# Kernel optimization log

Hardware: AMD Instinct MI355X
Metric: run time of the kernel (lower is better)

Reference implementation:

```python
import jax, jax.numpy as jnp
import numpy as np

B, S, H, T, DI, HID, K, HEADS = 8, 1024, 768, 8, 64, 128, 8, 2
NEG = 1.0e12


def _build_adj(spans):
    # spans: [K,3] int; returns [K+1,K+1] edge multiplicity matrix (dst, src)
    s, e = spans[:, 0], spans[:, 1]
    same = (s[:, None] == s[None, :]) & (e[:, None] == e[None, :])
    # contain[i,j]: span i strictly contains span j (source appends this edge twice)
    contain = (s[:, None] <= s[None, :]) & (e[None, :] <= e[:, None]) & (~same)
    N = K + 1
    adj = jnp.eye(N, dtype=jnp.float32)                    # PyG add_self_loops
    adj = adj.at[1:, 0].add(1.0)                           # global -> span i
    adj = adj.at[0, 1:].add(1.0)                           # span i -> global
    adj = adj.at[1:, 1:].add(2.0 * contain.T.astype(jnp.float32))
    return adj


def _gat(x, adj, W, a_src, a_dst, b):
    # x [N,F]; adj [N,N] multiplicity with layout (dst, src). PyG GATConv math.
    N = x.shape[0]
    h = (x @ W).reshape(N, HEADS, -1)                      # [N,Hd,D]
    asrc = jnp.einsum('nhd,hd->nh', h, a_src)
    adst = jnp.einsum('nhd,hd->nh', h, a_dst)
    ee = jax.nn.leaky_relu(adst[:, None, :] + asrc[None, :, :], 0.2)  # [dst,src,Hd]
    logmult = jnp.where(adj > 0, jnp.log(jnp.maximum(adj, 1e-20)), 0.0)
    scores = jnp.where(adj[:, :, None] > 0, ee + logmult[:, :, None], -1e30)
    attn = jax.nn.softmax(scores, axis=1)                  # softmax over source nodes
    out = jnp.einsum('dsh,shf->dhf', attn, h).reshape(N, -1)
    return out + b


def _layernorm(x, g, bta):
    mu = x.mean(-1, keepdims=True)
    var = x.var(-1, keepdims=True)
    return (x - mu) / jnp.sqrt(var + 1e-5) * g + bta


def _forward(hidden, attention_mask, spans, W1, a_src1, a_dst1, b1, ln_g, ln_b,
             W2, a_src2, a_dst2, b2, dense_W, dense_b,
             g_centers, g_sigmas, g_weights, corr):
    start, end, etype = spans[..., 0], spans[..., 1], spans[..., 2]  # [B,K]
    pos = jnp.arange(S)
    span_mask = ((pos[None, None, :] >= start[..., None]) &
                 (pos[None, None, :] <= end[..., None])).astype(hidden.dtype)  # [B,K,S]
    span_len = (end - start + 1).astype(hidden.dtype)
    span_feat = jnp.einsum('bks,bsh->bkh', span_mask, hidden) / span_len[..., None]
    global_feat = hidden.mean(axis=1, keepdims=True)                 # [B,1,H]
    nodes = jnp.concatenate([global_feat, span_feat], axis=1)        # [B,K+1,H]
    adj = jax.vmap(_build_adj)(spans)                                # [B,K+1,K+1]

    g1 = jax.vmap(lambda x, a: _gat(x, a, W1, a_src1, a_dst1, b1))(nodes, adj)
    g1 = _layernorm(jax.nn.relu(g1), ln_g, ln_b)
    g2 = jax.vmap(lambda x, a: _gat(x, a, W2, a_src2, a_dst2, b2))(g1, adj)
    g2 = jax.nn.relu(g2)
    enhanced = g2.mean(axis=1)                                       # per-graph mean pool [B,2*HID]

    cover = span_mask.sum(axis=1)                                    # [B,S] how many spans cover token s
    token_enh = cover[..., None] * enhanced[:, None, :]              # [B,S,2*HID]
    combined = jnp.concatenate([hidden, token_enh], axis=-1)

    qk = (combined @ dense_W + dense_b).reshape(B, S, T, 2 * DI)
    qw, kw = qk[..., :DI], qk[..., DI:]

    # RoPE (sin/cos interleaved exactly as in source)
    inv = jnp.power(10000.0, -2.0 * jnp.arange(DI // 2) / DI)
    ang = pos[:, None].astype(jnp.float32) * inv[None, :]            # [S,DI/2]
    sin = jnp.repeat(jnp.sin(ang), 2, axis=-1)[None, :, None, :]     # [1,S,1,DI]
    cos = jnp.repeat(jnp.cos(ang), 2, axis=-1)[None, :, None, :]

    def rot(v):
        v2 = jnp.stack([-v[..., 1::2], v[..., ::2]], axis=-1).reshape(v.shape)
        return v * cos + v2 * sin

    qw, kw = rot(qw), rot(kw)

    logits = jnp.einsum('bmtd,bntd->btmn', qw, kw)                   # [B,T,S,S]

    # multi-modal gaussian kernel span maps (vectorized over batch/span/component)
    pf = pos.astype(jnp.float32)
    dxs = pf[None, None, None, :] - start[..., None, None] - g_centers[None, None, :, None]
    dxe = pf[None, None, None, :] - end[..., None, None] - g_centers[None, None, :, None]
    Ksr = g_weights[None, None, :, None] * jnp.exp(-0.5 * (dxs / g_sigmas[None, None, :, None]) ** 2)
    Ken = g_weights[None, None, :, None] * jnp.exp(-0.5 * (dxe / g_sigmas[None, None, :, None]) ** 2)
    gmap = jnp.einsum('bkcm,bkcn->bkmn', Ksr, Ken)                   # [B,K,S,S]
    corr_span = corr[etype]                                          # [B,K,T]
    logits = logits + jnp.einsum('bkt,bkmn->btmn', corr_span, gmap)

    pad = attention_mask[:, None, None, :]                           # key-dim-only mask (as in source)
    logits = logits * pad - (1.0 - pad) * NEG
    tril = jnp.tril(jnp.ones((S, S), logits.dtype), -1)
    logits = logits - tril * NEG
    return logits / jnp.sqrt(jnp.float32(DI))


def setup_inputs() -> dict:
    key = jax.random.key(0)
    ks = jax.random.split(key, 16)
    hidden = jax.random.normal(ks[0], (B, S, H), jnp.float32)
    attention_mask = jnp.ones((B, S), jnp.float32)
    start = jax.random.randint(ks[1], (B, K), 0, S - 32)
    length = jax.random.randint(ks[2], (B, K), 1, 16)
    spans = jnp.stack([start, start + length,
                       jax.random.randint(ks[3], (B, K), 0, T)], axis=-1).astype(jnp.int32)
    sd = 0.05
    return {
        'hidden': hidden,
        'attention_mask': attention_mask,
        'spans': spans,
        'W1': jax.random.normal(ks[4], (H, HEADS * HID), jnp.float32) * sd,
        'a_src1': jax.random.normal(ks[5], (HEADS, HID), jnp.float32) * sd,
        'a_dst1': jax.random.normal(ks[6], (HEADS, HID), jnp.float32) * sd,
        'b1': jnp.zeros((HEADS * HID,), jnp.float32),
        'ln_g': jnp.ones((HEADS * HID,), jnp.float32),
        'ln_b': jnp.zeros((HEADS * HID,), jnp.float32),
        'W2': jax.random.normal(ks[7], (HEADS * HID, HEADS * HID), jnp.float32) * sd,
        'a_src2': jax.random.normal(ks[8], (HEADS, HID), jnp.float32) * sd,
        'a_dst2': jax.random.normal(ks[9], (HEADS, HID), jnp.float32) * sd,
        'b2': jnp.zeros((HEADS * HID,), jnp.float32),
        'dense_W': jax.random.normal(ks[10], (H + HEADS * HID, T * 2 * DI), jnp.float32) * sd,
        'dense_b': jnp.zeros((T * 2 * DI,), jnp.float32),
        'g_centers': jnp.array([0.0, 0.0], jnp.float32),
        'g_sigmas': jnp.array([1.0, 3.0], jnp.float32),
        'g_weights': jnp.array([0.5, 0.5], jnp.float32),
        'corr': jnp.eye(T, dtype=jnp.float32),
    }


def reference(hidden, attention_mask, spans, W1, a_src1, a_dst1, b1, ln_g, ln_b,
              W2, a_src2, a_dst2, b2, dense_W, dense_b,
              g_centers, g_sigmas, g_weights, corr):
    return _forward(hidden, attention_mask, spans, W1, a_src1, a_dst1, b1, ln_g, ln_b,
                    W2, a_src2, a_dst2, b2, dense_W, dense_b,
                    g_centers, g_sigmas, g_weights, corr)
```

## Files before the change

### kernel.cpp

```cpp
#include <hip/hip_runtime.h>
#include <cstdint>
#include <cstddef>

#define BB 8
#define SS 1024
#define HH 768
#define TT 8
#define DII 64
#define HIDD 128
#define KSP 8
#define NHEADS 2
#define NNODES 9
#define GDIM 256
#define CDIM 1024
#define DAUGP 96
#define NEGV 1e12f

using bf16x8 = __attribute__((ext_vector_type(8))) __bf16;
using f32x4  = __attribute__((ext_vector_type(4))) float;

static __device__ inline unsigned short f2bf(float x) {
  union { float f; unsigned u; } v; v.f = x;
  unsigned r = v.u + 0x7fff + ((v.u >> 16) & 1);
  return (unsigned short)(r >> 16);
}

__global__ __launch_bounds__(256) void kprep(
    const float* __restrict__ hidden, const float* __restrict__ dense_W,
    const int* __restrict__ spans, const float* __restrict__ corr,
    const float* __restrict__ gc, const float* __restrict__ gs,
    const float* __restrict__ gw,
    unsigned short* __restrict__ hbf, unsigned short* __restrict__ WtopT,
    float* __restrict__ part, float* __restrict__ nodes, float* __restrict__ cover,
    unsigned short* __restrict__ Qa, unsigned short* __restrict__ Ka) {
  int blk = blockIdx.x, tid = threadIdx.x;
  if (blk < 128) {
    int z = blk & 15, b = blk >> 4;
    const float* hb = hidden + (size_t)b * SS * HH;
    unsigned short* ho = hbf + (size_t)b * SS * HH;
    #pragma unroll
    for (int j = 0; j < 3; j++) {
      int c = tid + j * 256;
      float acc = 0.f;
      #pragma unroll 8
      for (int r = z * 64; r < z * 64 + 64; r++) {
        float v = hb[(size_t)r * HH + c];
        ho[(size_t)r * HH + c] = f2bf(v);
        acc += v;
      }
      part[((size_t)b * 16 + z) * HH + c] = acc;
    }
  } else if (blk < 192) {
    int q = blk - 128;
    int k = q & 7, b = q >> 3;
    __shared__ int sp[KSP * 3];
    if (tid < KSP * 3) sp[tid] = spans[b * KSP * 3 + tid];
    __syncthreads();
    if (tid < 128) {
      int s = k * 128 + tid;
      float c = 0.f;
      #pragma unroll
      for (int kk = 0; kk < KSP; kk++)
        c += (s >= sp[kk * 3] && s <= sp[kk * 3 + 1]) ? 1.f : 0.f;
      cover[b * SS + s] = c;
    }
    int st = sp[k * 3], en = sp[k * 3 + 1];
    float inv = 1.f / (float)(en - st + 1);
    const float* hb = hidden + (size_t)b * SS * HH;
    #pragma unroll
    for (int ci = 0; ci < 3; ci++) {
      int c = tid + ci * 256;
      float a = 0.f;
      #pragma unroll
      for (int j = 0; j < 16; j++) {
        int s = st + j;
        int sc = (s <= en) ? s : en;
        float v = hb[(size_t)sc * HH + c];
        a += (s <= en) ? v : 0.f;
      }
      nodes[((size_t)b * NNODES + (k + 1)) * HH + c] = a * inv;
    }
  } else if (blk < 960) {
    __shared__ float t[32][33];
    int q = blk - 192;
    int k0 = (q % 24) * 32, n0 = (q / 24) * 32;
    int r = tid >> 3, c4 = (tid & 7) * 4;
    float4 v = *(const float4*)&dense_W[(size_t)(k0 + r) * CDIM + n0 + c4];
    t[r][c4 + 0] = v.x; t[r][c4 + 1] = v.y; t[r][c4 + 2] = v.z; t[r][c4 + 3] = v.w;
    __syncthreads();
    int ro = tid >> 3, co4 = (tid & 7) * 4;
    ushort4 o;
    o.x = f2bf(t[co4 + 0][ro]); o.y = f2bf(t[co4 + 1][ro]);
    o.z = f2bf(t[co4 + 2][ro]); o.w = f2bf(t[co4 + 3][ro]);
    *(ushort4*)&WtopT[(size_t)(n0 + ro) * HH + k0 + co4] = o;
  } else {
    int g = tid >> 5, lane = tid & 31;
    int row = (blk - 960) * 8 + g;
    int b = row >> 10, s = row & 1023;
    int j = lane & 15;
    int kp = j >> 1, c = j & 1;
    int st = spans[(b * KSP + kp) * 3 + 0];
    int en = spans[(b * KSP + kp) * 3 + 1];
    int et = spans[(b * KSP + kp) * 3 + 2];
    float sig = gs[c], wgt = gw[c], ce = gc[c];
    if (lane < 16) {
      float dx = ((float)(s - st) - ce) / sig;
      float e = wgt * __expf(-0.5f * dx * dx);
      #pragma unroll
      for (int t = 0; t < TT; t++) {
        size_t base = ((size_t)(b * TT + t) * SS + s) * DAUGP;
        Qa[base + 64 + j] = f2bf(corr[et * TT + t] * e);
        Qa[base + 80 + j] = 0;
      }
    } else {
      float dx = ((float)(s - en) - ce) / sig;
      unsigned short bv = f2bf(wgt * __expf(-0.5f * dx * dx));
      #pragma unroll
      for (int t = 0; t < TT; t++) {
        size_t base = ((size_t)(b * TT + t) * SS + s) * DAUGP;
        Ka[base + 64 + j] = bv;
        Ka[base + 80 + j] = 0;
      }
    }
  }
}

__global__ __launch_bounds__(512) void k2_gat(
    const float* __restrict__ part, const float* __restrict__ nodes_g,
    const int* __restrict__ spans,
    const float* __restrict__ W1, const float* __restrict__ a_src1,
    const float* __restrict__ a_dst1, const float* __restrict__ b1,
    const float* __restrict__ ln_g, const float* __restrict__ ln_b,
    const float* __restrict__ W2, const float* __restrict__ a_src2,
    const float* __restrict__ a_dst2, const float* __restrict__ b2,
    float* __restrict__ enhg) {
  int b = blockIdx.x, tid = threadIdx.x;
  __shared__ __align__(16) float nod[NNODES * HH];
  __shared__ __align__(16) float hbuf[NNODES * GDIM];
  __shared__ __align__(16) float gbuf[NNODES * GDIM];
  __shared__ __align__(16) float pbuf[2 * NNODES * GDIM];
  __shared__ float asrc[NNODES * NHEADS], adst[NNODES * NHEADS];
  __shared__ float adjm[NNODES * NNODES];
  __shared__ float attn[NNODES * NNODES * NHEADS];
  __shared__ float mu_s[NNODES], rs_s[NNODES];
  __shared__ int sp[KSP * 3];
  if (tid < KSP * 3) sp[tid] = spans[b * KSP * 3 + tid];
  for (int c = tid; c < HH; c += 512) {
    float s = 0.f;
    #pragma unroll
    for (int z = 0; z < 16; z++) s += part[((size_t)b * 16 + z) * HH + c];
    nod[c] = s * (1.f / (float)SS);
  }
  for (int i = tid; i < (NNODES - 1) * HH; i += 512)
    nod[HH + i] = nodes_g[(size_t)b * NNODES * HH + HH + i];
  __syncthreads();
  {
    int col = tid & 255, h = tid >> 8;
    float acc[NNODES];
    #pragma unroll
    for (int n = 0; n < NNODES; n++) acc[n] = 0.f;
    int dlo = h * 384;
    #pragma unroll 2
    for (int d0 = dlo; d0 < dlo + 384; d0 += 4) {
      float4 nv[NNODES];
      #pragma unroll
      for (int n = 0; n < NNODES; n++) nv[n] = *(const float4*)&nod[n * HH + d0];
      float w0 = W1[(size_t)(d0 + 0) * GDIM + col];
      float w1 = W1[(size_t)(d0 + 1) * GDIM + col];
      float w2 = W1[(size_t)(d0 + 2) * GDIM + col];
      float w3 = W1[(size_t)(d0 + 3) * GDIM + col];
      #pragma unroll
      for (int n = 0; n < NNODES; n++)
        acc[n] += nv[n].x * w0 + nv[n].y * w1 + nv[n].z * w2 + nv[n].w * w3;
    }
    #pragma unroll
    for (int n = 0; n < NNODES; n++) pbuf[(h * NNODES + n) * GDIM + col] = acc[n];
  }
  __syncthreads();
  if (tid < GDIM) {
    #pragma unroll
    for (int n = 0; n < NNODES; n++)
      hbuf[n * GDIM + tid] = pbuf[n * GDIM + tid] + pbuf[(NNODES + n) * GDIM + tid];
  } else if (tid < 256 + NNODES * NNODES) {
    int q = tid - 256;
    int i = q / NNODES, j = q % NNODES;
    float a = (i == j) ? 1.f : 0.f;
    if (i > 0 && j == 0) a += 1.f;
    if (i == 0 && j > 0) a += 1.f;
    if (i > 0 && j > 0 && i != j) {
      int x = j - 1, y = i - 1;
      int sx = sp[x * 3], ex = sp[x * 3 + 1], sy = sp[y * 3], ey = sp[y * 3 + 1];
      bool same = (sx == sy) && (ex == ey);
      if (sx <= sy && ey <= ex && !same) a += 2.f;
    }
    adjm[q] = a;
  }
  __syncthreads();
  if (tid < NNODES * NHEADS) {
    int n = tid >> 1, hd = tid & 1;
    float sa = 0.f, sd = 0.f;
    #pragma unroll 8
    for (int f = 0; f < HIDD; f++) {
      float v = hbuf[n * GDIM + hd * HIDD + f];
      sa += v * a_src1[hd * HIDD + f];
      sd += v * a_dst1[hd * HIDD + f];
    }
    asrc[tid] = sa; adst[tid] = sd;
  }
  __syncthreads();
  if (tid < NNODES * NHEADS) {
    int d = tid >> 1, hd = tid & 1;
    float sc[NNODES]; float mx = -1e30f;
    for (int s2 = 0; s2 < NNODES; s2++) {
      float a = adjm[d * NNODES + s2]; float v;
      if (a > 0.f) {
        float e = adst[d * 2 + hd] + asrc[s2 * 2 + hd];
        e = (e > 0.f) ? e : 0.2f * e;
        v = e + __logf(a);
      } else v = -1e30f;
      sc[s2] = v; mx = fmaxf(mx, v);
    }
    float ssum = 0.f;
    for (int s2 = 0; s2 < NNODES; s2++) { float ex = __expf(sc[s2] - mx); sc[s2] = ex; ssum += ex; }
    float inv = 1.f / ssum;
    for (int s2 = 0; s2 < NNODES; s2++) attn[(d * NNODES + s2) * NHEADS + hd] = sc[s2] * inv;
  }
  __syncthreads();
  if (tid < 256) {
    int hd = tid >> 7;
    float bbv = b1[tid];
    for (int d = 0; d < NNODES; d++) {
      float acc = bbv;
      #pragma unroll
      for (int s2 = 0; s2 < NNODES; s2++)
        acc += attn[(d * NNODES + s2) * NHEADS + hd] * hbuf[s2 * GDIM + tid];
      gbuf[d * GDIM + tid] = fmaxf(acc, 0.f);
    }
  }
  __syncthreads();
  if (tid < NNODES) {
    float s1 = 0.f, s2v = 0.f;
    #pragma unroll 8
    for (int o = 0; o < GDIM; o++) { float v = gbuf[tid * GDIM + o]; s1 += v; s2v += v * v; }
    float mu = s1 / (float)GDIM;
    float var = s2v / (float)GDIM - mu * mu;
    mu_s[tid] = mu; rs_s[tid] = rsqrtf(var + 1e-5f);
  }
  __syncthreads();
  if (tid < 256) {
    float g = ln_g[tid], bt = ln_b[tid];
    for (int d = 0; d < NNODES; d++)
      gbuf[d * GDIM + tid] = (gbuf[d * GDIM + tid] - mu_s[d]) * rs_s[d] * g + bt;
  }
  __syncthreads();
  {
    int col = tid & 255, h = tid >> 8;
    float acc[NNODES];
    #pragma unroll
    for (int n = 0; n < NNODES; n++) acc[n] = 0.f;
    int dlo = h * 128;
    #pragma unroll 2
    for (int d0 = dlo; d0 < dlo + 128; d0 += 4) {
      float4 nv[NNODES];
      #pragma unroll
      for (int n = 0; n < NNODES; n++) nv[n] = *(const float4*)&gbuf[n * GDIM + d0];
      float w0 = W2[(size_t)(d0 + 0) * GDIM + col];
      float w1 = W2[(size_t)(d0 + 1) * GDIM + col];
      float w2 = W2[(size_t)(d0 + 2) * GDIM + col];
      float w3 = W2[(size_t)(d0 + 3) * GDIM + col];
      #pragma unroll
      for (int n = 0; n < NNODES; n++)
        acc[n] += nv[n].x * w0 + nv[n].y * w1 + nv[n].z * w2 + nv[n].w * w3;
    }
    #pragma unroll
    for (int n = 0; n < NNODES; n++) pbuf[(h * NNODES + n) * GDIM + col] = acc[n];
  }
  __syncthreads();
  if (tid < GDIM) {
    #pragma unroll
    for (int n = 0; n < NNODES; n++)
      hbuf[n * GDIM + tid] = pbuf[n * GDIM + tid] + pbuf[(NNODES + n) * GDIM + tid];
  }
  __syncthreads();
  if (tid < NNODES * NHEADS) {
    int n = tid >> 1, hd = tid & 1;
    float sa = 0.f, sd = 0.f;
    #pragma unroll 8
    for (int f = 0; f < HIDD; f++) {
      float v = hbuf[n * GDIM + hd * HIDD + f];
      sa += v * a_src2[hd * HIDD + f];
      sd += v * a_dst2[hd * HIDD + f];
    }
    asrc[tid] = sa; adst[tid] = sd;
  }
  __syncthreads();
  if (tid < NNODES * NHEADS) {
    int d = tid >> 1, hd = tid & 1;
    float sc[NNODES]; float mx = -1e30f;
    for (int s2 = 0; s2 < NNODES; s2++) {
      float a = adjm[d * NNODES + s2]; float v;
      if (a > 0.f) {
        float e = adst[d * 2 + hd] + asrc[s2 * 2 + hd];
        e = (e > 0.f) ? e : 0.2f * e;
        v = e + __logf(a);
      } else v = -1e30f;
      sc[s2] = v; mx = fmaxf(mx, v);
    }
    float ssum = 0.f;
    for (int s2 = 0; s2 < NNODES; s2++) { float ex = __expf(sc[s2] - mx); sc[s2] = ex; ssum += ex; }
    float inv = 1.f / ssum;
    for (int s2 = 0; s2 < NNODES; s2++) attn[(d * NNODES + s2) * NHEADS + hd] = sc[s2] * inv;
  }
  __syncthreads();
  if (tid < 256) {
    int hd = tid >> 7;
    float bbv = b2[tid];
    float msum = 0.f;
    for (int d = 0; d < NNODES; d++) {
      float acc = bbv;
      #pragma unroll
      for (int s2 = 0; s2 < NNODES; s2++)
        acc += attn[(d * NNODES + s2) * NHEADS + hd] * hbuf[s2 * GDIM + tid];
      msum += fmaxf(acc, 0.f);
    }
    enhg[b * GDIM + tid] = msum / 9.f;
  }
}

__global__ void k2b_e2(const float* __restrict__ enhg, const float* __restrict__ dense_W,
                       float* __restrict__ E2) {
  int b = blockIdx.y, tid = threadIdx.x;
  int o = blockIdx.x * 256 + tid;
  __shared__ __align__(16) float eh[GDIM];
  eh[tid] = enhg[b * GDIM + tid];
  __syncthreads();
  float acc = 0.f;
  #pragma unroll 2
  for (int d = 0; d < GDIM; d += 4) {
    float4 ev = *(const float4*)&eh[d];
    acc += ev.x * dense_W[(size_t)(HH + d + 0) * CDIM + o];
    acc += ev.y * dense_W[(size_t)(HH + d + 1) * CDIM + o];
    acc += ev.z * dense_W[(size_t)(HH + d + 2) * CDIM + o];
    acc += ev.w * dense_W[(size_t)(HH + d + 3) * CDIM + o];
  }
  E2[b * CDIM + o] = acc;
}

__global__ __launch_bounds__(256) void k3_dense(
    const unsigned short* __restrict__ hbf, const unsigned short* __restrict__ WtopT,
    const float* __restrict__ dense_b, const float* __restrict__ cover,
    const float* __restrict__ E2,
    unsigned short* __restrict__ Qa, unsigned short* __restrict__ Ka) {
  __shared__ unsigned short As[128 * 40];
  __shared__ unsigned short Bs[128 * 40];
  int tid = threadIdx.x;
  int n0 = blockIdx.x * 128, m0 = blockIdx.y * 128;
  int wave = tid >> 6, lane = tid & 63;
  int wr = wave >> 1, wc = wave & 1;
  int colL = lane & 15, quad = lane >> 4;
  f32x4 acc[4][4];
  #pragma unroll
  for (int i = 0; i < 4; i++)
    #pragma unroll
    for (int j = 0; j < 4; j++) { acc[i][j][0] = 0.f; acc[i][j][1] = 0.f; acc[i][j][2] = 0.f; acc[i][j][3] = 0.f; }
  for (int k0 = 0; k0 < HH; k0 += 32) {
    uint4 va[2], vb[2];
    #pragma unroll
    for (int it = 0; it < 2; it++) {
      int idx = tid + it * 256;
      int r = idx >> 2, seg = idx & 3;
      va[it] = *(const uint4*)(hbf + (size_t)(m0 + r) * HH + k0 + seg * 8);
      vb[it] = *(const uint4*)(WtopT + (size_t)(n0 + r) * HH + k0 + seg * 8);
    }
    __syncthreads();
    #pragma unroll
    for (int it = 0; it < 2; it++) {
      int idx = tid + it * 256;
      int r = idx >> 2, seg = idx & 3;
      *(uint4*)&As[r * 40 + seg * 8] = va[it];
      *(uint4*)&Bs[r * 40 + seg * 8] = vb[it];
    }
    __syncthreads();
    bf16x8 af[4], bf[4];
    #pragma unroll
    for (int tm = 0; tm < 4; tm++)
      af[tm] = *(const bf16x8*)&As[(wr * 64 + tm * 16 + colL) * 40 + quad * 8];
    #pragma unroll
    for (int tn = 0; tn < 4; tn++)
      bf[tn] = *(const bf16x8*)&Bs[(wc * 64 + tn * 16 + colL) * 40 + quad * 8];
    #pragma unroll
    for (int tm = 0; tm < 4; tm++)
      #pragma unroll
      for (int tn = 0; tn < 4; tn++)
        acc[tm][tn] = __builtin_amdgcn_mfma_f32_16x16x32_bf16(af[tm], bf[tn], acc[tm][tn], 0, 0, 0);
  }
  int b = m0 >> 10;
  const float LOG1E4_32 = 0.28782313662425576f;
  unsigned short* __restrict__ dst = (wc == 0) ? Qa : Ka;
  #pragma unroll
  for (int tn = 0; tn < 4; tn++) {
    int col = n0 + wc * 64 + tn * 16 + colL;
    float e2 = E2[b * CDIM + col];
    float db = dense_b[col];
    int t = col >> 7;
    int dd = tn * 16 + colL;
    int i0 = dd >> 1;
    float inv = __expf(-(float)i0 * LOG1E4_32);
    float sgn = (dd & 1) ? 1.f : -1.f;
    size_t tbase = (size_t)(b * TT + t) * SS;
    #pragma unroll
    for (int tm = 0; tm < 4; tm++) {
      int rbase = m0 + wr * 64 + tm * 16 + quad * 4;
      #pragma unroll
      for (int r = 0; r < 4; r++) {
        int m = rbase + r;
        int s = m & 1023;
        float w = acc[tm][tn][r] + cover[m] * e2 + db;
        float p = __shfl_xor(w, 1, 64);
        float sn, cs;
        __sincosf((float)s * inv, &sn, &cs);
        float o = w * cs + sgn * p * sn;
        dst[(tbase + s) * DAUGP + dd] = f2bf(o);
      }
    }
  }
}

__global__ __launch_bounds__(256) void k5_logits(
    const unsigned short* __restrict__ Qa, const unsigned short* __restrict__ Ka,
    const float* __restrict__ amask, float* __restrict__ out) {
  int bz = blockIdx.z; int b = bz >> 3;
  int n0 = blockIdx.x * 128, m0 = blockIdx.y * 128;
  int tid = threadIdx.x;
  if (n0 + 127 < m0) {
    int r0 = tid >> 5, c4 = (tid & 31) * 4;
    float4 pv = *(const float4*)&amask[b * SS + n0 + c4];
    float4 o;
    o.x = (-(1.f - pv.x) * NEGV - NEGV) * 0.125f;
    o.y = (-(1.f - pv.y) * NEGV - NEGV) * 0.125f;
    o.z = (-(1.f - pv.z) * NEGV - NEGV) * 0.125f;
    o.w = (-(1.f - pv.w) * NEGV - NEGV) * 0.125f;
    for (int r = r0; r < 128; r += 8)
      *(float4*)&out[((size_t)bz * SS + m0 + r) * SS + n0 + c4] = o;
    return;
  }
  __shared__ unsigned short Qs[128 * 104];
  __shared__ unsigned short Ks[128 * 104];
  const unsigned short* Qrow = Qa + ((size_t)bz * SS + m0) * DAUGP;
  const unsigned short* Krow = Ka + ((size_t)bz * SS + n0) * DAUGP;
  #pragma unroll
  for (int it = 0; it < 6; it++) {
    int idx = tid + it * 256;
    int r = idx / 12, seg = idx % 12;
    uint4 vq = *(const uint4*)(Qrow + (size_t)r * DAUGP + seg * 8);
    uint4 vk = *(const uint4*)(Krow + (size_t)r * DAUGP + seg * 8);
    *(uint4*)&Qs[r * 104 + seg * 8] = vq;
    *(uint4*)&Ks[r * 104 + seg * 8] = vk;
  }
  __syncthreads();
  int wave = tid >> 6, lane = tid & 63;
  int wr = wave >> 1, wc = wave & 1;
  int colL = lane & 15, quad = lane >> 4;
  f32x4 acc[4][4];
  #pragma unroll
  for (int i = 0; i < 4; i++)
    #pragma unroll
    for (int j = 0; j < 4; j++) { acc[i][j][0] = 0.f; acc[i][j][1] = 0.f; acc[i][j][2] = 0.f; acc[i][j][3] = 0.f; }
  #pragma unroll
  for (int ks = 0; ks < 3; ks++) {
    bf16x8 af[4], bf[4];
    #pragma unroll
    for (int tm = 0; tm < 4; tm++)
      af[tm] = *(const bf16x8*)&Qs[(wr * 64 + tm * 16 + colL) * 104 + ks * 32 + quad * 8];
    #pragma unroll
    for (int tn = 0; tn < 4; tn++)
      bf[tn] = *(const bf16x8*)&Ks[(wc * 64 + tn * 16 + colL) * 104 + ks * 32 + quad * 8];
    #pragma unroll
    for (int tm = 0; tm < 4; tm++)
      #pragma unroll
      for (int tn = 0; tn < 4; tn++)
        acc[tm][tn] = __builtin_amdgcn_mfma_f32_16x16x32_bf16(af[tm], bf[tn], acc[tm][tn], 0, 0, 0);
  }
  #pragma unroll
  for (int tn = 0; tn < 4; tn++) {
    int col = n0 + wc * 64 + tn * 16 + colL;
    float p = amask[b * SS + col];
    float negp = -(1.f - p) * NEGV;
    #pragma unroll
    for (int tm = 0; tm < 4; tm++) {
      int rbase = m0 + wr * 64 + tm * 16 + quad * 4;
      #pragma unroll
      for (int r = 0; r < 4; r++) {
        int m = rbase + r;
        float v = acc[tm][tn][r] * p + negp;
        if (col < m) v -= NEGV;
        out[((size_t)bz * SS + m) * SS + col] = v * 0.125f;
      }
    }
  }
}

extern "C" void kernel_launch(void* const* d_in, const int* in_sizes, int n_in,
                              void* d_out, int out_size, void* d_ws, size_t ws_size,
                              hipStream_t stream) {
  const float* hidden  = (const float*)d_in[0];
  const float* amask   = (const float*)d_in[1];
  const int*   spans   = (const int*)d_in[2];
  const float* W1      = (const float*)d_in[3];
  const float* a_src1  = (const float*)d_in[4];
  const float* a_dst1  = (const float*)d_in[5];
  const float* b1      = (const float*)d_in[6];
  const float* ln_g    = (const float*)d_in[7];
  const float* ln_b    = (const float*)d_in[8];
  const float* W2      = (const float*)d_in[9];
  const float* a_src2  = (const float*)d_in[10];
  const float* a_dst2  = (const float*)d_in[11];
  const float* b2      = (const float*)d_in[12];
  const float* dense_W = (const float*)d_in[13];
  const float* dense_b = (const float*)d_in[14];
  const float* gc      = (const float*)d_in[15];
  const float* gs      = (const float*)d_in[16];
  const float* gw      = (const float*)d_in[17];
  const float* corr    = (const float*)d_in[18];

  char* wsb = (char*)d_ws;
  unsigned short* hbf  = (unsigned short*)wsb;                wsb += (size_t)BB * SS * HH * 2;
  unsigned short* WtopT= (unsigned short*)wsb;                wsb += (size_t)CDIM * HH * 2;
  unsigned short* Qa   = (unsigned short*)wsb;                wsb += (size_t)BB * TT * SS * DAUGP * 2;
  unsigned short* Ka   = (unsigned short*)wsb;                wsb += (size_t)BB * TT * SS * DAUGP * 2;
  float* nodes         = (float*)wsb;                         wsb += (size_t)BB * NNODES * HH * 4;
  float* cover         = (float*)wsb;                         wsb += (size_t)BB * SS * 4;
  float* E2            = (float*)wsb;                         wsb += (size_t)BB * CDIM * 4;
  float* enhg          = (float*)wsb;                         wsb += (size_t)BB * GDIM * 4;
  float* part          = (float*)wsb;                         wsb += (size_t)BB * 16 * HH * 4;
  float* outp = (float*)d_out;

  kprep<<<1984, 256, 0, stream>>>(hidden, dense_W, spans, corr, gc, gs, gw,
                                  hbf, WtopT, part, nodes, cover, Qa, Ka);
  k2_gat<<<BB, 512, 0, stream>>>(part, nodes, spans, W1, a_src1, a_dst1, b1, ln_g, ln_b,
                                 W2, a_src2, a_dst2, b2, enhg);
  k2b_e2<<<dim3(CDIM / 256, BB), 256, 0, stream>>>(enhg, dense_W, E2);
  k3_dense<<<dim3(CDIM / 128, (BB * SS) / 128), 256, 0, stream>>>(hbf, WtopT, dense_b,
                                                                  cover, E2, Qa, Ka);
  k5_logits<<<dim3(8, 8, BB * TT), 256, 0, stream>>>(Qa, Ka, amask, outp);
}
```

Baseline: 554.6 us.

## Stage logits tile through LDS for coalesced stores; widen GAT block to 1024 threads

The logits kernel now writes each 64x128 half of its output tile into shared memory, reusing the Q/K staging buffer, and then stores it with contiguous float4 row writes. Before, each lane scattered scalar stores along the MFMA accumulator layout. The GAT kernel also doubles its block to 1024 threads and splits both projection reductions four ways, adding more partial sums to combine. The change costs extra barriers and an LDS round trip in the logits epilogue, in exchange for better-coalesced writes of the large output.

New measurement: 556.3 us. About the same (+0.3%).

```diff
diff --git a/kernel.cpp b/kernel.cpp
--- a/kernel.cpp
+++ b/kernel.cpp
@@ -125,7 +125,7 @@
   }
 }
 
-__global__ __launch_bounds__(512) void k2_gat(
+__global__ __launch_bounds__(1024) void k2_gat(
     const float* __restrict__ part, const float* __restrict__ nodes_g,
     const int* __restrict__ spans,
     const float* __restrict__ W1, const float* __restrict__ a_src1,
@@ -138,30 +138,30 @@
   __shared__ __align__(16) float nod[NNODES * HH];
   __shared__ __align__(16) float hbuf[NNODES * GDIM];
   __shared__ __align__(16) float gbuf[NNODES * GDIM];
-  __shared__ __align__(16) float pbuf[2 * NNODES * GDIM];
+  __shared__ __align__(16) float pbuf[4 * NNODES * GDIM];
   __shared__ float asrc[NNODES * NHEADS], adst[NNODES * NHEADS];
   __shared__ float adjm[NNODES * NNODES];
   __shared__ float attn[NNODES * NNODES * NHEADS];
   __shared__ float mu_s[NNODES], rs_s[NNODES];
   __shared__ int sp[KSP * 3];
   if (tid < KSP * 3) sp[tid] = spans[b * KSP * 3 + tid];
-  for (int c = tid; c < HH; c += 512) {
+  for (int c = tid; c < HH; c += 1024) {
     float s = 0.f;
     #pragma unroll
     for (int z = 0; z < 16; z++) s += part[((size_t)b * 16 + z) * HH + c];
     nod[c] = s * (1.f / (float)SS);
   }
-  for (int i = tid; i < (NNODES - 1) * HH; i += 512)
+  for (int i = tid; i < (NNODES - 1) * HH; i += 1024)
     nod[HH + i] = nodes_g[(size_t)b * NNODES * HH + HH + i];
   __syncthreads();
   {
-    int col = tid & 255, h = tid >> 8;
+    int col = tid & 255, q = tid >> 8;
     float acc[NNODES];
     #pragma unroll
     for (int n = 0; n < NNODES; n++) acc[n] = 0.f;
-    int dlo = h * 384;
+    int dlo = q * 192;
     #pragma unroll 2
-    for (int d0 = dlo; d0 < dlo + 384; d0 += 4) {
+    for (int d0 = dlo; d0 < dlo + 192; d0 += 4) {
       float4 nv[NNODES];
       #pragma unroll
       for (int n = 0; n < NNODES; n++) nv[n] = *(const float4*)&nod[n * HH + d0];
@@ -174,13 +174,15 @@
         acc[n] += nv[n].x * w0 + nv[n].y * w1 + nv[n].z * w2 + nv[n].w * w3;
     }
     #pragma unroll
-    for (int n = 0; n < NNODES; n++) pbuf[(h * NNODES + n) * GDIM + col] = acc[n];
+    for (int n = 0; n < NNODES; n++) pbuf[(q * NNODES + n) * GDIM + col] = acc[n];
   }
   __syncthreads();
   if (tid < GDIM) {
     #pragma unroll
     for (int n = 0; n < NNODES; n++)
-      hbuf[n * GDIM + tid] = pbuf[n * GDIM + tid] + pbuf[(NNODES + n) * GDIM + tid];
+      hbuf[n * GDIM + tid] = pbuf[n * GDIM + tid] + pbuf[(NNODES + n) * GDIM + tid]
+                           + pbuf[(2 * NNODES + n) * GDIM + tid]
+                           + pbuf[(3 * NNODES + n) * GDIM + tid];
   } else if (tid < 256 + NNODES * NNODES) {
     int q = tid - 256;
     int i = q / NNODES, j = q % NNODES;
@@ -254,13 +256,13 @@
   }
   __syncthreads();
   {
-    int col = tid & 255, h = tid >> 8;
+    int col = tid & 255, q = tid >> 8;
     float acc[NNODES];
     #pragma unroll
     for (int n = 0; n < NNODES; n++) acc[n] = 0.f;
-    int dlo = h * 128;
+    int dlo = q * 64;
     #pragma unroll 2
-    for (int d0 = dlo; d0 < dlo + 128; d0 += 4) {
+    for (int d0 = dlo; d0 < dlo + 64; d0 += 4) {
       float4 nv[NNODES];
       #pragma unroll
       for (int n = 0; n < NNODES; n++) nv[n] = *(const float4*)&gbuf[n * GDIM + d0];
@@ -273,13 +275,15 @@
         acc[n] += nv[n].x * w0 + nv[n].y * w1 + nv[n].z * w2 + nv[n].w * w3;
     }
     #pragma unroll
-    for (int n = 0; n < NNODES; n++) pbuf[(h * NNODES + n) * GDIM + col] = acc[n];
+    for (int n = 0; n < NNODES; n++) pbuf[(q * NNODES + n) * GDIM + col] = acc[n];
   }
   __syncthreads();
   if (tid < GDIM) {
     #pragma unroll
     for (int n = 0; n < NNODES; n++)
-      hbuf[n * GDIM + tid] = pbuf[n * GDIM + tid] + pbuf[(NNODES + n) * GDIM + tid];
+      hbuf[n * GDIM + tid] = pbuf[n * GDIM + tid] + pbuf[(NNODES + n) * GDIM + tid]
+                           + pbuf[(2 * NNODES + n) * GDIM + tid]
+                           + pbuf[(3 * NNODES + n) * GDIM + tid];
   }
   __syncthreads();
   if (tid < NNODES * NHEADS) {
@@ -444,8 +448,9 @@
       *(float4*)&out[((size_t)bz * SS + m0 + r) * SS + n0 + c4] = o;
     return;
   }
-  __shared__ unsigned short Qs[128 * 104];
-  __shared__ unsigned short Ks[128 * 104];
+  __shared__ __align__(16) unsigned short QKs[2 * 128 * 104];
+  unsigned short* Qs = QKs;
+  unsigned short* Ks = QKs + 128 * 104;
   const unsigned short* Qrow = Qa + ((size_t)bz * SS + m0) * DAUGP;
   const unsigned short* Krow = Ka + ((size_t)bz * SS + n0) * DAUGP;
   #pragma unroll
@@ -481,22 +486,36 @@
       for (int tn = 0; tn < 4; tn++)
         acc[tm][tn] = __builtin_amdgcn_mfma_f32_16x16x32_bf16(af[tm], bf[tn], acc[tm][tn], 0, 0, 0);
   }
+  float* Cs = (float*)QKs;
   #pragma unroll
-  for (int tn = 0; tn < 4; tn++) {
-    int col = n0 + wc * 64 + tn * 16 + colL;
-    float p = amask[b * SS + col];
-    float negp = -(1.f - p) * NEGV;
-    #pragma unroll
-    for (int tm = 0; tm < 4; tm++) {
-      int rbase = m0 + wr * 64 + tm * 16 + quad * 4;
-      #pragma unroll
-      for (int r = 0; r < 4; r++) {
-        int m = rbase + r;
-        float v = acc[tm][tn][r] * p + negp;
-        if (col < m) v -= NEGV;
-        out[((size_t)bz * SS + m) * SS + col] = v * 0.125f;
+  for (int h = 0; h < 2; h++) {
+    __syncthreads();
+    if (wr == h) {
+      #pragma unroll
+      for (int tn = 0; tn < 4; tn++) {
+        int cloc = wc * 64 + tn * 16 + colL;
+        float p = amask[b * SS + n0 + cloc];
+        float negp = -(1.f - p) * NEGV;
+        #pragma unroll
+        for (int tm = 0; tm < 4; tm++) {
+          int rloc = tm * 16 + quad * 4;
+          #pragma unroll
+          for (int r = 0; r < 4; r++) {
+            int m = m0 + h * 64 + rloc + r;
+            float v = acc[tm][tn][r] * p + negp;
+            if (n0 + cloc < m) v -= NEGV;
+            Cs[(rloc + r) * 132 + cloc] = v * 0.125f;
+          }
+        }
       }
     }
+    __syncthreads();
+    int row = tid >> 2, seg = tid & 3;
+    const float* src = &Cs[row * 132 + seg * 32];
+    float* dstp = &out[((size_t)bz * SS + m0 + h * 64 + row) * SS + n0 + seg * 32];
+    #pragma unroll
+    for (int j = 0; j < 8; j++)
+      *(float4*)(dstp + j * 4) = *(const float4*)(src + j * 4);
   }
 }
 
@@ -537,8 +556,8 @@
 
   kprep<<<1984, 256, 0, stream>>>(hidden, dense_W, spans, corr, gc, gs, gw,
                                   hbf, WtopT, part, nodes, cover, Qa, Ka);
-  k2_gat<<<BB, 512, 0, stream>>>(part, nodes, spans, W1, a_src1, a_dst1, b1, ln_g, ln_b,
-                                 W2, a_src2, a_dst2, b2, enhg);
+  k2_gat<<<BB, 1024, 0, stream>>>(part, nodes, spans, W1, a_src1, a_dst1, b1, ln_g, ln_b,
+                                  W2, a_src2, a_dst2, b2, enhg);
   k2b_e2<<<dim3(CDIM / 256, BB), 256, 0, stream>>>(enhg, dense_W, E2);
   k3_dense<<<dim3(CDIM / 128, (BB * SS) / 128), 256, 0, stream>>>(hbf, WtopT, dense_b,
                                                                   cover, E2, Qa, Ka);
```
